# Optimization experiments

Hardware: AMD Instinct MI355X
Metric: run time of the kernel (lower is better)

The kernel has to match this reference:

```python
import jax, jax.numpy as jnp
import numpy as np

T_LEN, E_LEN, BATCH, DIM = 32, 256, 16, 512  # topic_len, exp_len, batch, input=hidden size
HID = 512


def setup_inputs() -> dict:
    key = jax.random.key(0)
    k1, k2, k3, k4, k5, k6 = jax.random.split(key, 6)
    topic = jax.random.normal(k1, (T_LEN, BATCH, DIM), dtype=jnp.float32)
    exp_output = jax.random.normal(k2, (E_LEN, BATCH, DIM), dtype=jnp.float32)
    seq_mask = jax.random.bernoulli(k3, 0.1, (E_LEN, BATCH))  # True = masked exp position
    # nn.Linear(hidden+input, hidden): weight [HID, HID+DIM], bias [HID]
    lim1 = 1.0 / np.sqrt(HID + DIM)
    W_attn = jax.random.uniform(k4, (HID, HID + DIM), minval=-lim1, maxval=lim1, dtype=jnp.float32)
    b_attn = jax.random.uniform(k5, (HID,), minval=-lim1, maxval=lim1, dtype=jnp.float32)
    # nn.Linear(hidden, 1): weight [1, HID], bias [1]
    lim2 = 1.0 / np.sqrt(HID)
    kv, kb = jax.random.split(k6)
    v_score = jax.random.uniform(kv, (1, HID), minval=-lim2, maxval=lim2, dtype=jnp.float32)
    b_score = jax.random.uniform(kb, (1,), minval=-lim2, maxval=lim2, dtype=jnp.float32)
    return {"topic": topic, "exp_output": exp_output, "seq_mask": seq_mask,
            "W_attn": W_attn, "b_attn": b_attn, "v_score": v_score, "b_score": b_score}


def reference(topic, exp_output, seq_mask, W_attn, b_attn, v_score, b_score):
    # topic: [T, B, D]; exp_output: [E, B, D]; seq_mask: [E, B] bool
    D = topic.shape[2]
    # Split the concat-Linear: cat(topic, exp) @ W.T == topic @ W[:, :D].T + exp @ W[:, D:].T
    proj_t = jnp.einsum('tbd,hd->bth', topic, W_attn[:, :D])        # [B, T, H]
    proj_e = jnp.einsum('ebd,hd->beh', exp_output, W_attn[:, D:])   # [B, E, H]
    feat = jnp.tanh(proj_t[:, :, None, :] + proj_e[:, None, :, :] + b_attn)  # [B, T, E, H]
    energies = jnp.einsum('bteh,h->bte', feat, v_score[0]) + b_score[0]      # [B, T, E]
    # mask exp positions (broadcast over topic dim), as masked_fill(-1e12)
    energies = jnp.where(seq_mask.T[:, None, :], jnp.float32(-1e12), energies)
    attn_s1 = jax.nn.softmax(jnp.swapaxes(energies, 1, 2), axis=2)  # [B, E, T], softmax over topics
    attn_s2 = jax.nn.softmax(energies, axis=2)                      # [B, T, E], softmax over exp
    new_exp = jnp.einsum('bet,btd->bed', attn_s1, jnp.swapaxes(topic, 0, 1))       # [B, E, D]
    new_topic = jnp.einsum('bte,bed->btd', attn_s2, jnp.swapaxes(exp_output, 0, 1))  # [B, T, D]
    return new_topic, new_exp
```

## Files before the change

kernel.cpp:

```cpp
#include <hip/hip_runtime.h>
#include <hip/hip_bf16.h>
#include <cstddef>
#include <cstdint>

#define T_LEN 32
#define E_LEN 256
#define BATCH 16
#define DIM 512
#define HID 512
#define WROW 1024

#define TWO_LOG2E 2.8853900817779268f

typedef __attribute__((ext_vector_type(8))) short bf16x8;
typedef __attribute__((ext_vector_type(4))) float f32x4;

__device__ inline bf16x8 cvt8(float4 a, float4 b) {
    union { bf16x8 v; __hip_bfloat16 h[8]; } u;
    u.h[0] = __float2bfloat16(a.x); u.h[1] = __float2bfloat16(a.y);
    u.h[2] = __float2bfloat16(a.z); u.h[3] = __float2bfloat16(a.w);
    u.h[4] = __float2bfloat16(b.x); u.h[5] = __float2bfloat16(b.y);
    u.h[6] = __float2bfloat16(b.z); u.h[7] = __float2bfloat16(b.w);
    return u.v;
}

#define GPAD 8
#define GLDR (64 + GPAD)

__global__ __launch_bounds__(256) void gemm_fused(
    const float* __restrict__ topic, const float* __restrict__ expo,
    const float* __restrict__ W, const float* __restrict__ battn,
    float* __restrict__ PT, float* __restrict__ PE) {
    __shared__ __hip_bfloat16 As[64 * GLDR];
    __shared__ __hip_bfloat16 Bs[64 * GLDR];
    const int tid = threadIdx.x;
    const int by = blockIdx.y;
    const float* A; const float* Wp; const float* bias; float* C; int m0;
    if (by < 8) { A = topic; Wp = W;       bias = battn;   C = PT; m0 = by * 64; }
    else        { A = expo;  Wp = W + DIM; bias = nullptr; C = PE; m0 = (by - 8) * 64; }
    const int n0 = blockIdx.x * 64;
    const int w = tid >> 6;
    const int lane = tid & 63;
    const int l15 = lane & 15;
    const int g = lane >> 4;
    const int srow = tid >> 2;
    const int sc = tid & 3;

    f32x4 acc[4];
    const f32x4 z = {0.f, 0.f, 0.f, 0.f};
#pragma unroll
    for (int nt = 0; nt < 4; ++nt) acc[nt] = z;

    const float* ga = A + (size_t)(m0 + srow) * 512 + sc * 8;
    const float* gb = Wp + (size_t)(n0 + srow) * WROW + sc * 8;

    float4 a0 = *(const float4*)(ga);
    float4 a1 = *(const float4*)(ga + 4);
    float4 a2 = *(const float4*)(ga + 32);
    float4 a3 = *(const float4*)(ga + 36);
    float4 b0 = *(const float4*)(gb);
    float4 b1 = *(const float4*)(gb + 4);
    float4 b2 = *(const float4*)(gb + 32);
    float4 b3 = *(const float4*)(gb + 36);

    for (int kk = 0; kk < 8; ++kk) {
        bf16x8 av0 = cvt8(a0, a1), av1 = cvt8(a2, a3);
        bf16x8 bv0 = cvt8(b0, b1), bv1 = cvt8(b2, b3);
        if (kk < 7) {
            ga += 64; gb += 64;
            a0 = *(const float4*)(ga);
            a1 = *(const float4*)(ga + 4);
            a2 = *(const float4*)(ga + 32);
            a3 = *(const float4*)(ga + 36);
            b0 = *(const float4*)(gb);
            b1 = *(const float4*)(gb + 4);
            b2 = *(const float4*)(gb + 32);
            b3 = *(const float4*)(gb + 36);
        }
        __syncthreads();
        *(bf16x8*)&As[srow * GLDR + sc * 8] = av0;
        *(bf16x8*)&As[srow * GLDR + sc * 8 + 32] = av1;
        *(bf16x8*)&Bs[srow * GLDR + sc * 8] = bv0;
        *(bf16x8*)&Bs[srow * GLDR + sc * 8 + 32] = bv1;
        __syncthreads();
#pragma unroll
        for (int s = 0; s < 2; ++s) {
            bf16x8 af = *(const bf16x8*)&As[(w * 16 + l15) * GLDR + (s * 4 + g) * 8];
#pragma unroll
            for (int nt = 0; nt < 4; ++nt) {
                bf16x8 bf = *(const bf16x8*)&Bs[(nt * 16 + l15) * GLDR + (s * 4 + g) * 8];
                acc[nt] = __builtin_amdgcn_mfma_f32_16x16x32_bf16(af, bf, acc[nt], 0, 0, 0);
            }
        }
    }
#pragma unroll
    for (int nt = 0; nt < 4; ++nt) {
        int n = n0 + nt * 16 + l15;
        float bv = bias ? bias[n] : 0.f;
#pragma unroll
        for (int r = 0; r < 4; ++r) {
            int m = m0 + w * 16 + g * 4 + r;
            C[(size_t)m * 512 + n] = (acc[nt][r] + bv) * TWO_LOG2E;
        }
    }
}

__global__ __launch_bounds__(256) void energies_k(const float* __restrict__ PT,
                                                  const float* __restrict__ PE,
                                                  const float* __restrict__ v,
                                                  const float* __restrict__ bscore,
                                                  const int* __restrict__ mask,
                                                  float* __restrict__ EN) {
    const int b = blockIdx.x;
    const int tg = blockIdx.y;
    const int ech = blockIdx.z;
    const int lane = threadIdx.x & 63;
    const int w = threadIdx.x >> 6;
    const int h0 = lane * 8;

    float sv[8], spt[4][8];
    float sumv;
    {
        float4 v0 = *(const float4*)(v + h0);
        float4 v1 = *(const float4*)(v + h0 + 4);
        float vr[8] = {v0.x, v0.y, v0.z, v0.w, v1.x, v1.y, v1.z, v1.w};
        float s = 0.f;
#pragma unroll
        for (int j = 0; j < 8; ++j) { sv[j] = -2.f * vr[j]; s += vr[j]; }
#pragma unroll
        for (int off = 32; off; off >>= 1) s += __shfl_xor(s, off);
        sumv = s;
#pragma unroll
        for (int i = 0; i < 4; ++i) {
            const float* p = PT + ((size_t)((tg * 4 + i) * BATCH + b)) * HID + h0;
            float4 p0 = *(const float4*)(p);
            float4 p1 = *(const float4*)(p + 4);
            spt[i][0] = p0.x; spt[i][1] = p0.y; spt[i][2] = p0.z; spt[i][3] = p0.w;
            spt[i][4] = p1.x; spt[i][5] = p1.y; spt[i][6] = p1.z; spt[i][7] = p1.w;
        }
    }
    const int e0 = ech * 16 + w * 4;
    const float bs = bscore[0];
#pragma unroll
    for (int ei = 0; ei < 4; ++ei) {
        const int e = e0 + ei;
        const float* pe = PE + ((size_t)(e * BATCH + b)) * HID + h0;
        float4 p0 = *(const float4*)(pe);
        float4 p1 = *(const float4*)(pe + 4);
        float pr[8] = {p0.x, p0.y, p0.z, p0.w, p1.x, p1.y, p1.z, p1.w};
        float acc[4] = {0.f, 0.f, 0.f, 0.f};
#pragma unroll
        for (int i = 0; i < 4; ++i) {
#pragma unroll
            for (int j = 0; j < 8; ++j) {
                float x = spt[i][j] + pr[j];
                float ex = __builtin_amdgcn_exp2f(x);
                float r = __builtin_amdgcn_rcpf(ex + 1.f);
                acc[i] = fmaf(sv[j], r, acc[i]);
            }
        }
#pragma unroll
        for (int i = 0; i < 4; ++i) {
#pragma unroll
            for (int off = 32; off; off >>= 1) acc[i] += __shfl_xor(acc[i], off);
        }
        if (lane == 0) {
            const int msk = mask[e * BATCH + b];
#pragma unroll
            for (int i = 0; i < 4; ++i) {
                float en = sumv + bs + acc[i];
                if (msk != 0) en = -1e12f;
                EN[((size_t)b * T_LEN + tg * 4 + i) * E_LEN + e] = en;
            }
        }
    }
}

__global__ __launch_bounds__(256) void epilogue_k(const float* __restrict__ EN,
                                                  const float* __restrict__ topic,
                                                  const float* __restrict__ expo,
                                                  float* __restrict__ out) {
    const int tid = threadIdx.x;
    if (blockIdx.x < 1024) {
        const int idx = blockIdx.x * 4 + (tid >> 6);
        const int b = idx >> 8;
        const int e = idx & 255;
        const int lane = tid & 63;
        float x = (lane < T_LEN) ? EN[((size_t)b * T_LEN + lane) * E_LEN + e] : -3e38f;
        float m = x;
#pragma unroll
        for (int off = 16; off; off >>= 1) m = fmaxf(m, __shfl_xor(m, off));
        float p = (lane < T_LEN) ? __expf(x - m) : 0.f;
        float s = p;
#pragma unroll
        for (int off = 16; off; off >>= 1) s += __shfl_xor(s, off);
        float wv = __fdividef(p, s);
        float4 acc0 = {0.f, 0.f, 0.f, 0.f};
        float4 acc1 = {0.f, 0.f, 0.f, 0.f};
        const int d0 = lane * 8;
        for (int t = 0; t < T_LEN; ++t) {
            const float wt = __shfl(wv, t);
            const float* row = topic + ((size_t)t * BATCH + b) * DIM + d0;
            float4 r0 = *(const float4*)(row);
            float4 r1 = *(const float4*)(row + 4);
            acc0.x = fmaf(wt, r0.x, acc0.x); acc0.y = fmaf(wt, r0.y, acc0.y);
            acc0.z = fmaf(wt, r0.z, acc0.z); acc0.w = fmaf(wt, r0.w, acc0.w);
            acc1.x = fmaf(wt, r1.x, acc1.x); acc1.y = fmaf(wt, r1.y, acc1.y);
            acc1.z = fmaf(wt, r1.z, acc1.z); acc1.w = fmaf(wt, r1.w, acc1.w);
        }
        float* o = out + (size_t)BATCH * T_LEN * DIM + ((size_t)b * E_LEN + e) * DIM + d0;
        *(float4*)(o) = acc0;
        *(float4*)(o + 4) = acc1;
    } else {
        const int q = blockIdx.x - 1024;
        const int bt = q >> 1;
        const int half = q & 1;
        __shared__ float wsm[E_LEN];
        __shared__ float wred[4];
        float x = EN[(size_t)bt * E_LEN + tid];
        const int lane = tid & 63;
        const int wid = tid >> 6;
        float m = x;
#pragma unroll
        for (int off = 32; off; off >>= 1) m = fmaxf(m, __shfl_xor(m, off));
        if (lane == 0) wred[wid] = m;
        __syncthreads();
        m = fmaxf(fmaxf(wred[0], wred[1]), fmaxf(wred[2], wred[3]));
        float p = __expf(x - m);
        float s = p;
#pragma unroll
        for (int off = 32; off; off >>= 1) s += __shfl_xor(s, off);
        __syncthreads();
        if (lane == 0) wred[wid] = s;
        __syncthreads();
        s = wred[0] + wred[1] + wred[2] + wred[3];
        wsm[tid] = __fdividef(p, s);
        __syncthreads();
        const int b = bt >> 5;
        const float* base = expo + half * 256 + tid;
        float acc = 0.f;
#pragma unroll 8
        for (int e = 0; e < E_LEN; ++e) {
            float rv = base[(size_t)(e * BATCH + b) * DIM];
            acc = fmaf(wsm[e], rv, acc);
        }
        out[(size_t)bt * DIM + half * 256 + tid] = acc;
    }
}

extern "C" void kernel_launch(void* const* d_in, const int* in_sizes, int n_in,
                              void* d_out, int out_size, void* d_ws, size_t ws_size,
                              hipStream_t stream) {
    const float* topic = (const float*)d_in[0];
    const float* expo  = (const float*)d_in[1];
    const int*   mask  = (const int*)d_in[2];
    const float* W     = (const float*)d_in[3];
    const float* battn = (const float*)d_in[4];
    const float* vsc   = (const float*)d_in[5];
    const float* bsc   = (const float*)d_in[6];
    float* out = (float*)d_out;

    float* PT = (float*)d_ws;
    float* PE = PT + (size_t)T_LEN * BATCH * HID;
    float* EN = PE + (size_t)E_LEN * BATCH * HID;

    gemm_fused<<<dim3(8, 72), 256, 0, stream>>>(topic, expo, W, battn, PT, PE);
    energies_k<<<dim3(BATCH, 8, 16), 256, 0, stream>>>(PT, PE, vsc, bsc, mask, EN);
    epilogue_k<<<2048, 256, 0, stream>>>(EN, topic, expo, out);
}
```

Baseline: 129.6 us.

## Precompute exp2 of projections in GEMM and restructure epilogue with shared-memory reuse

The GEMM epilogue now stores exp2 of each scaled projection, so the energies inner loop replaces exp2(a+b) with a product a*b+1 followed by a reciprocal, dropping one transcendental per (t,e,h) element. The epilogue kernel is reorganised: the exp-side path processes 4 exp positions per wave and stages topic rows in shared memory for reuse, and the topic-side path handles 4 topics per block so each exp row load feeds four accumulators. Grid size shrinks from 2048 to 512 blocks. Precomputed exponentials can overflow for large projections, which changes numerical behaviour compared with the additive form.

```diff
diff --git a/kernel.cpp b/kernel.cpp
--- a/kernel.cpp
+++ b/kernel.cpp
@@ -30,14 +30,14 @@
 __global__ __launch_bounds__(256) void gemm_fused(
     const float* __restrict__ topic, const float* __restrict__ expo,
     const float* __restrict__ W, const float* __restrict__ battn,
-    float* __restrict__ PT, float* __restrict__ PE) {
+    float* __restrict__ EPT, float* __restrict__ EPE) {
     __shared__ __hip_bfloat16 As[64 * GLDR];
     __shared__ __hip_bfloat16 Bs[64 * GLDR];
     const int tid = threadIdx.x;
     const int by = blockIdx.y;
     const float* A; const float* Wp; const float* bias; float* C; int m0;
-    if (by < 8) { A = topic; Wp = W;       bias = battn;   C = PT; m0 = by * 64; }
-    else        { A = expo;  Wp = W + DIM; bias = nullptr; C = PE; m0 = (by - 8) * 64; }
+    if (by < 8) { A = topic; Wp = W;       bias = battn;   C = EPT; m0 = by * 64; }
+    else        { A = expo;  Wp = W + DIM; bias = nullptr; C = EPE; m0 = (by - 8) * 64; }
     const int n0 = blockIdx.x * 64;
     const int w = tid >> 6;
     const int lane = tid & 63;
@@ -100,13 +100,13 @@
 #pragma unroll
         for (int r = 0; r < 4; ++r) {
             int m = m0 + w * 16 + g * 4 + r;
-            C[(size_t)m * 512 + n] = (acc[nt][r] + bv) * TWO_LOG2E;
-        }
-    }
-}
-
-__global__ __launch_bounds__(256) void energies_k(const float* __restrict__ PT,
-                                                  const float* __restrict__ PE,
+            C[(size_t)m * 512 + n] = __builtin_amdgcn_exp2f((acc[nt][r] + bv) * TWO_LOG2E);
+        }
+    }
+}
+
+__global__ __launch_bounds__(256) void energies_k(const float* __restrict__ EPT,
+                                                  const float* __restrict__ EPE,
                                                   const float* __restrict__ v,
                                                   const float* __restrict__ bscore,
                                                   const int* __restrict__ mask,
@@ -132,7 +132,7 @@
         sumv = s;
 #pragma unroll
         for (int i = 0; i < 4; ++i) {
-            const float* p = PT + ((size_t)((tg * 4 + i) * BATCH + b)) * HID + h0;
+            const float* p = EPT + ((size_t)((tg * 4 + i) * BATCH + b)) * HID + h0;
             float4 p0 = *(const float4*)(p);
             float4 p1 = *(const float4*)(p + 4);
             spt[i][0] = p0.x; spt[i][1] = p0.y; spt[i][2] = p0.z; spt[i][3] = p0.w;
@@ -144,7 +144,7 @@
 #pragma unroll
     for (int ei = 0; ei < 4; ++ei) {
         const int e = e0 + ei;
-        const float* pe = PE + ((size_t)(e * BATCH + b)) * HID + h0;
+        const float* pe = EPE + ((size_t)(e * BATCH + b)) * HID + h0;
         float4 p0 = *(const float4*)(pe);
         float4 p1 = *(const float4*)(pe + 4);
         float pr[8] = {p0.x, p0.y, p0.z, p0.w, p1.x, p1.y, p1.z, p1.w};
@@ -153,9 +153,8 @@
         for (int i = 0; i < 4; ++i) {
 #pragma unroll
             for (int j = 0; j < 8; ++j) {
-                float x = spt[i][j] + pr[j];
-                float ex = __builtin_amdgcn_exp2f(x);
-                float r = __builtin_amdgcn_rcpf(ex + 1.f);
+                float q = fmaf(spt[i][j], pr[j], 1.0f);
+                float r = __builtin_amdgcn_rcpf(q);
                 acc[i] = fmaf(sv[j], r, acc[i]);
             }
         }
@@ -180,71 +179,116 @@
                                                   const float* __restrict__ topic,
                                                   const float* __restrict__ expo,
                                                   float* __restrict__ out) {
+    __shared__ float smem[4096];
     const int tid = threadIdx.x;
-    if (blockIdx.x < 1024) {
-        const int idx = blockIdx.x * 4 + (tid >> 6);
-        const int b = idx >> 8;
-        const int e = idx & 255;
-        const int lane = tid & 63;
-        float x = (lane < T_LEN) ? EN[((size_t)b * T_LEN + lane) * E_LEN + e] : -3e38f;
-        float m = x;
-#pragma unroll
-        for (int off = 16; off; off >>= 1) m = fmaxf(m, __shfl_xor(m, off));
-        float p = (lane < T_LEN) ? __expf(x - m) : 0.f;
-        float s = p;
-#pragma unroll
-        for (int off = 16; off; off >>= 1) s += __shfl_xor(s, off);
-        float wv = __fdividef(p, s);
-        float4 acc0 = {0.f, 0.f, 0.f, 0.f};
-        float4 acc1 = {0.f, 0.f, 0.f, 0.f};
+    const int lane = tid & 63;
+    const int w = tid >> 6;
+    if (blockIdx.x < 256) {
+        const int b = blockIdx.x >> 4;
+        const int e0 = (blockIdx.x & 15) * 16 + w * 4;
+        float wv[4];
+#pragma unroll
+        for (int ei = 0; ei < 4; ++ei) {
+            const int e = e0 + ei;
+            float x = (lane < T_LEN) ? EN[((size_t)b * T_LEN + lane) * E_LEN + e] : -3e38f;
+            float m = x;
+#pragma unroll
+            for (int off = 16; off; off >>= 1) m = fmaxf(m, __shfl_xor(m, off));
+            float p = (lane < T_LEN) ? __expf(x - m) : 0.f;
+            float s = p;
+#pragma unroll
+            for (int off = 16; off; off >>= 1) s += __shfl_xor(s, off);
+            wv[ei] = __fdividef(p, s);
+        }
+        float acc[4][8] = {};
         const int d0 = lane * 8;
-        for (int t = 0; t < T_LEN; ++t) {
-            const float wt = __shfl(wv, t);
-            const float* row = topic + ((size_t)t * BATCH + b) * DIM + d0;
-            float4 r0 = *(const float4*)(row);
-            float4 r1 = *(const float4*)(row + 4);
-            acc0.x = fmaf(wt, r0.x, acc0.x); acc0.y = fmaf(wt, r0.y, acc0.y);
-            acc0.z = fmaf(wt, r0.z, acc0.z); acc0.w = fmaf(wt, r0.w, acc0.w);
-            acc1.x = fmaf(wt, r1.x, acc1.x); acc1.y = fmaf(wt, r1.y, acc1.y);
-            acc1.z = fmaf(wt, r1.z, acc1.z); acc1.w = fmaf(wt, r1.w, acc1.w);
-        }
-        float* o = out + (size_t)BATCH * T_LEN * DIM + ((size_t)b * E_LEN + e) * DIM + d0;
-        *(float4*)(o) = acc0;
-        *(float4*)(o + 4) = acc1;
+        for (int tc = 0; tc < 4; ++tc) {
+            __syncthreads();
+            {
+                int f = tid * 16;
+                int r = f >> 9;
+                int d = f & 511;
+                const float* src = topic + ((size_t)(tc * 8 + r) * BATCH + b) * DIM + d;
+                float4 s0 = *(const float4*)(src);
+                float4 s1 = *(const float4*)(src + 4);
+                float4 s2 = *(const float4*)(src + 8);
+                float4 s3 = *(const float4*)(src + 12);
+                *(float4*)&smem[r * 512 + d] = s0;
+                *(float4*)&smem[r * 512 + d + 4] = s1;
+                *(float4*)&smem[r * 512 + d + 8] = s2;
+                *(float4*)&smem[r * 512 + d + 12] = s3;
+            }
+            __syncthreads();
+#pragma unroll
+            for (int t8 = 0; t8 < 8; ++t8) {
+                const int t = tc * 8 + t8;
+                float4 r0 = *(const float4*)&smem[t8 * 512 + d0];
+                float4 r1 = *(const float4*)&smem[t8 * 512 + d0 + 4];
+                float wt[4];
+#pragma unroll
+                for (int ei = 0; ei < 4; ++ei) wt[ei] = __shfl(wv[ei], t);
+#pragma unroll
+                for (int ei = 0; ei < 4; ++ei) {
+                    acc[ei][0] = fmaf(wt[ei], r0.x, acc[ei][0]);
+                    acc[ei][1] = fmaf(wt[ei], r0.y, acc[ei][1]);
+                    acc[ei][2] = fmaf(wt[ei], r0.z, acc[ei][2]);
+                    acc[ei][3] = fmaf(wt[ei], r0.w, acc[ei][3]);
+                    acc[ei][4] = fmaf(wt[ei], r1.x, acc[ei][4]);
+                    acc[ei][5] = fmaf(wt[ei], r1.y, acc[ei][5]);
+                    acc[ei][6] = fmaf(wt[ei], r1.z, acc[ei][6]);
+                    acc[ei][7] = fmaf(wt[ei], r1.w, acc[ei][7]);
+                }
+            }
+        }
+#pragma unroll
+        for (int ei = 0; ei < 4; ++ei) {
+            float* o = out + (size_t)BATCH * T_LEN * DIM +
+                       ((size_t)b * E_LEN + e0 + ei) * DIM + d0;
+            *(float4*)(o) = *(float4*)&acc[ei][0];
+            *(float4*)(o + 4) = *(float4*)&acc[ei][4];
+        }
     } else {
-        const int q = blockIdx.x - 1024;
-        const int bt = q >> 1;
+        const int q = blockIdx.x - 256;
+        const int b = q >> 5;
+        const int tg = (q >> 1) & 15;
+        const int bq = q >> 5;
+        const int tg8 = (q >> 2) & 7;
         const int half = q & 1;
-        __shared__ float wsm[E_LEN];
-        __shared__ float wred[4];
-        float x = EN[(size_t)bt * E_LEN + tid];
-        const int lane = tid & 63;
-        const int wid = tid >> 6;
-        float m = x;
+        const int bb = q >> 4;
+        const int tgq = (q >> 1) & 7;
+        const int hf = q & 1;
+        (void)b; (void)tg; (void)bq; (void)tg8; (void)half;
+        const int t = tgq * 4 + w;
+        const int bt = bb * T_LEN + t;
+        float4 xv = *(const float4*)&EN[(size_t)bt * E_LEN + lane * 4];
+        float m = fmaxf(fmaxf(xv.x, xv.y), fmaxf(xv.z, xv.w));
 #pragma unroll
         for (int off = 32; off; off >>= 1) m = fmaxf(m, __shfl_xor(m, off));
-        if (lane == 0) wred[wid] = m;
+        float p0 = __expf(xv.x - m), p1 = __expf(xv.y - m);
+        float p2 = __expf(xv.z - m), p3 = __expf(xv.w - m);
+        float s = p0 + p1 + p2 + p3;
+#pragma unroll
+        for (int off = 32; off; off >>= 1) s += __shfl_xor(s, off);
+        float inv = __fdividef(1.f, s);
+        float4 wvv = {p0 * inv, p1 * inv, p2 * inv, p3 * inv};
+        *(float4*)&smem[w * 256 + lane * 4] = wvv;
         __syncthreads();
-        m = fmaxf(fmaxf(wred[0], wred[1]), fmaxf(wred[2], wred[3]));
-        float p = __expf(x - m);
-        float s = p;
-#pragma unroll
-        for (int off = 32; off; off >>= 1) s += __shfl_xor(s, off);
-        __syncthreads();
-        if (lane == 0) wred[wid] = s;
-        __syncthreads();
-        s = wred[0] + wred[1] + wred[2] + wred[3];
-        wsm[tid] = __fdividef(p, s);
-        __syncthreads();
-        const int b = bt >> 5;
-        const float* base = expo + half * 256 + tid;
-        float acc = 0.f;
+        const int dglob = hf * 256 + tid;
+        const float* base = expo + (size_t)bb * DIM + dglob;
+        float a0 = 0.f, a1 = 0.f, a2 = 0.f, a3 = 0.f;
 #pragma unroll 8
         for (int e = 0; e < E_LEN; ++e) {
-            float rv = base[(size_t)(e * BATCH + b) * DIM];
-            acc = fmaf(wsm[e], rv, acc);
-        }
-        out[(size_t)bt * DIM + half * 256 + tid] = acc;
+            float rv = base[(size_t)e * BATCH * DIM];
+            a0 = fmaf(smem[e], rv, a0);
+            a1 = fmaf(smem[256 + e], rv, a1);
+            a2 = fmaf(smem[512 + e], rv, a2);
+            a3 = fmaf(smem[768 + e], rv, a3);
+        }
+        float* o = out + ((size_t)bb * T_LEN + tgq * 4) * DIM + dglob;
+        o[0] = a0;
+        o[DIM] = a1;
+        o[2 * DIM] = a2;
+        o[3 * DIM] = a3;
     }
 }
 
@@ -260,11 +304,11 @@
     const float* bsc   = (const float*)d_in[6];
     float* out = (float*)d_out;
 
-    float* PT = (float*)d_ws;
-    float* PE = PT + (size_t)T_LEN * BATCH * HID;
-    float* EN = PE + (size_t)E_LEN * BATCH * HID;
-
-    gemm_fused<<<dim3(8, 72), 256, 0, stream>>>(topic, expo, W, battn, PT, PE);
-    energies_k<<<dim3(BATCH, 8, 16), 256, 0, stream>>>(PT, PE, vsc, bsc, mask, EN);
-    epilogue_k<<<2048, 256, 0, stream>>>(EN, topic, expo, out);
-}
+    float* EPT = (float*)d_ws;
+    float* EPE = EPT + (size_t)T_LEN * BATCH * HID;
+    float* EN  = EPE + (size_t)E_LEN * BATCH * HID;
+
+    gemm_fused<<<dim3(8, 72), 256, 0, stream>>>(topic, expo, W, battn, EPT, EPE);
+    energies_k<<<dim3(BATCH, 8, 16), 256, 0, stream>>>(EPT, EPE, vsc, bsc, mask, EN);
+    epilogue_k<<<512, 256, 0, stream>>>(EN, topic, expo, out);
+}
```

New measurement: 120.3 us. 1.08x faster.
